# Performance work log

Hardware: AMD Instinct MI355X
Metric: run time of the kernel (lower is better)

Reference implementation:

```python
import jax, jax.numpy as jnp
import numpy as np

D_MODEL = 1024
N_HEADS = 16
HEAD_DIM = D_MODEL // N_HEADS


def setup_inputs() -> dict:
    key = jax.random.key(0)
    ks = jax.random.split(key, 9)
    s = 1.0 / np.sqrt(D_MODEL)
    x = jax.random.normal(ks[0], (2, 2048, D_MODEL), dtype=jnp.float32)
    wq = jax.random.uniform(ks[1], (D_MODEL, D_MODEL), jnp.float32, -s, s)
    bq = jax.random.uniform(ks[2], (D_MODEL,), jnp.float32, -s, s)
    wk = jax.random.uniform(ks[3], (D_MODEL, D_MODEL), jnp.float32, -s, s)
    bk = jax.random.uniform(ks[4], (D_MODEL,), jnp.float32, -s, s)
    wv = jax.random.uniform(ks[5], (D_MODEL, D_MODEL), jnp.float32, -s, s)
    bv = jax.random.uniform(ks[6], (D_MODEL,), jnp.float32, -s, s)
    wo = jax.random.uniform(ks[7], (D_MODEL, D_MODEL), jnp.float32, -s, s)
    bo = jax.random.uniform(ks[8], (D_MODEL,), jnp.float32, -s, s)
    return {"x": x, "wq": wq, "bq": bq, "wk": wk, "bk": bk,
            "wv": wv, "bv": bv, "wo": wo, "bo": bo}


def reference(x, wq, bq, wk, bk, wv, bv, wo, bo):
    B, S, _ = x.shape
    scale = HEAD_DIM ** -0.5

    def proj(w, b):
        # torch Linear: x @ W^T + b, then split heads -> [B, H, S, Dh]
        y = jnp.einsum('bsd,ed->bse', x, w) + b
        return y.reshape(B, S, N_HEADS, HEAD_DIM).transpose(0, 2, 1, 3)

    q = proj(wq, bq)
    k = proj(wk, bk)
    v = proj(wv, bv)

    attn = jnp.einsum('bhqd,bhkd->bhqk', q, k) * scale  # [B,H,S,S]
    causal = jnp.triu(jnp.ones((S, S), dtype=bool), k=1)
    attn = jnp.where(causal, -jnp.inf, attn)
    attn = jax.nn.softmax(attn, axis=-1)
    out = jnp.einsum('bhqk,bhkd->bhqd', attn, v)
    out = out.transpose(0, 2, 1, 3).reshape(B, S, D_MODEL)
    return jnp.einsum('bsd,ed->bse', out, wo) + bo
```

## Files before the change

### kernel.cpp

```cpp
#include <hip/hip_runtime.h>
#include <hip/hip_bf16.h>

#define D_MODEL 1024
#define NHEADS  16
#define HDIM    64
#define SEQ     2048
#define BATCH   2
#define MROWS   (BATCH * SEQ)
#define CHELEM  ((size_t)BATCH * NHEADS * SEQ * HDIM)

typedef __bf16 bf16x8 __attribute__((ext_vector_type(8)));
typedef float  f32x4  __attribute__((ext_vector_type(4)));

__device__ __forceinline__ unsigned short f2bf(float f) {
  unsigned u = __builtin_bit_cast(unsigned, f);
  return (unsigned short)((u + 0x7fffu + ((u >> 16) & 1u)) >> 16);
}

__device__ __forceinline__ float fexp2(float x) {
#if __has_builtin(__builtin_amdgcn_exp2f)
  return __builtin_amdgcn_exp2f(x);
#else
  return __expf(x * 0.6931471805599453f);
#endif
}

__device__ __forceinline__ f32x4 mfma16(bf16x8 a, bf16x8 b, f32x4 c) {
  return __builtin_amdgcn_mfma_f32_16x16x32_bf16(a, b, c, 0, 0, 0);
}

__device__ __forceinline__ void gll16(const unsigned short* g, unsigned short* l) {
  __builtin_amdgcn_global_load_lds(
      (const __attribute__((address_space(1))) unsigned*)g,
      (__attribute__((address_space(3))) unsigned*)l, 16, 0, 0);
}

__global__ void cvt_f32_bf16(const float* __restrict__ in,
                             unsigned short* __restrict__ out, int n4) {
  int i = blockIdx.x * blockDim.x + threadIdx.x;
  if (i >= n4) return;
  float4 v = reinterpret_cast<const float4*>(in)[i];
  ushort4 o;
  o.x = f2bf(v.x); o.y = f2bf(v.y); o.z = f2bf(v.z); o.w = f2bf(v.w);
  reinterpret_cast<ushort4*>(out)[i] = o;
}

__global__ void cvt_w4(const float* __restrict__ s0, const float* __restrict__ s1,
                       const float* __restrict__ s2, const float* __restrict__ s3,
                       unsigned short* __restrict__ d0, unsigned short* __restrict__ d1,
                       unsigned short* __restrict__ d2, unsigned short* __restrict__ d3) {
  int i = blockIdx.x * blockDim.x + threadIdx.x;
  const int y = blockIdx.y;
  const float* s = (y == 0) ? s0 : (y == 1) ? s1 : (y == 2) ? s2 : s3;
  unsigned short* d = (y == 0) ? d0 : (y == 1) ? d1 : (y == 2) ? d2 : d3;
  float4 v = reinterpret_cast<const float4*>(s)[i];
  ushort4 o;
  o.x = f2bf(v.x); o.y = f2bf(v.y); o.z = f2bf(v.z); o.w = f2bf(v.w);
  reinterpret_cast<ushort4*>(d)[i] = o;
}

template <int MODE>
__global__ __launch_bounds__(256) void gemm_bt2(
    const unsigned short* __restrict__ A,
    const unsigned short* __restrict__ Bt,
    const float* __restrict__ b0, const float* __restrict__ b1,
    const float* __restrict__ b2,
    void* __restrict__ outp, int M, int N, int K) {
  __shared__ __align__(16) unsigned short lA[128 * 32];
  __shared__ __align__(16) unsigned short lB[128 * 32];
  const int tid = threadIdx.x;
  const int m0 = blockIdx.y * 128, n0 = blockIdx.x * 128;
  const int lane = tid & 63, wid = tid >> 6;
  const int wr = wid >> 1, wc = wid & 1;
  const int fr = lane & 15, g = lane >> 4;

  const int srow = wid * 32 + (lane >> 2);
  const int scol = ((lane & 3) ^ ((lane >> 3) & 3)) * 8;
  const unsigned short* gA = A + (size_t)(m0 + srow) * K + scol;
  const unsigned short* gB = Bt + (size_t)(n0 + srow) * K + scol;
  unsigned short* lAw = lA + wid * 1024;
  unsigned short* lBw = lB + wid * 1024;

  const int rswz = (g ^ ((fr >> 1) & 3)) * 8;

  f32x4 acc[4][4];
#pragma unroll
  for (int i = 0; i < 4; ++i)
#pragma unroll
    for (int j = 0; j < 4; ++j) acc[i][j] = (f32x4){0.f, 0.f, 0.f, 0.f};

  for (int kt = 0; kt < K; kt += 32) {
    gll16(gA + kt, lAw);
    gll16(gA + (size_t)16 * K + kt, lAw + 512);
    gll16(gB + kt, lBw);
    gll16(gB + (size_t)16 * K + kt, lBw + 512);
    __syncthreads();
    bf16x8 af[4], bfv[4];
#pragma unroll
    for (int i = 0; i < 4; ++i)
      af[i] = *reinterpret_cast<const bf16x8*>(
          &lA[(wr * 64 + i * 16 + fr) * 32 + rswz]);
#pragma unroll
    for (int j = 0; j < 4; ++j)
      bfv[j] = *reinterpret_cast<const bf16x8*>(
          &lB[(wc * 64 + j * 16 + fr) * 32 + rswz]);
#pragma unroll
    for (int i = 0; i < 4; ++i)
#pragma unroll
      for (int j = 0; j < 4; ++j)
        acc[i][j] = mfma16(af[i], bfv[j], acc[i][j]);
    __syncthreads();
  }

  const int src = n0 >> 10;
  const float* bp = (MODE == 2) ? b0 : (src == 0 ? b0 : (src == 1 ? b1 : b2));
#pragma unroll
  for (int i = 0; i < 4; ++i)
#pragma unroll
    for (int j = 0; j < 4; ++j)
#pragma unroll
      for (int r = 0; r < 4; ++r) {
        int m = m0 + wr * 64 + i * 16 + g * 4 + r;
        int n = n0 + wc * 64 + j * 16 + fr;
        if (MODE == 2) {
          float val = acc[i][j][r] + bp[n];
          reinterpret_cast<float*>(outp)[(size_t)m * N + n] = val;
        } else {
          int within = n & 1023;
          float val = acc[i][j][r] + bp[within];
          if (src == 0) val *= 0.1803368867f;
          int b = m >> 11, s = m & 2047;
          int hh = within >> 6, dh = within & 63;
          size_t idx;
          if (src != 2)
            idx = ((size_t)(b * NHEADS + hh) * SEQ + s) * HDIM + dh;
          else
            idx = ((size_t)(b * NHEADS + hh) * HDIM + dh) * SEQ + s;
          reinterpret_cast<unsigned short*>(outp)[(size_t)src * CHELEM + idx] =
              f2bf(val);
        }
      }
}

__global__ __launch_bounds__(256) void attn_fwd12(
    const unsigned short* __restrict__ Q,
    const unsigned short* __restrict__ Km,
    const unsigned short* __restrict__ Vt,
    unsigned short* __restrict__ O) {
  const int tid = threadIdx.x;
  const int lane = tid & 63, wid = tid >> 6;
  const int fr = lane & 15, g = lane >> 4;
  const int lin = blockIdx.x;
  const int c = lin & 7;
  const int t = lin >> 3;
  const int j = t & 15;
  const int sgrp = t >> 4;
  const int slab = sgrp * 8 + c;
  const int b = slab >> 4, h = slab & 15;
  const int bh = b * NHEADS + h;

  __shared__ __align__(16) unsigned short lK[2][4096];
  __shared__ __align__(16) unsigned short lV[2][4096];

  const unsigned short* kptr = Km + (size_t)bh * SEQ * HDIM;
  const unsigned short* vptr = Vt + (size_t)bh * HDIM * SEQ;

  const int sr0 = tid >> 3;
  const int sch = tid & 7;
  const int schx = ((sch ^ (sr0 & 7)) << 3);
  const int kswz0 = ((g ^ (fr & 7)) << 3);
  const int kswz1 = (((4 + g) ^ (fr & 7)) << 3);
  const int g2 = g >> 1, gh = (g & 1) * 4;
  const int vlo0 = (((0 + g2) ^ (fr & 7)) << 3) + gh;
  const int vhi0 = (((2 + g2) ^ (fr & 7)) << 3) + gh;
  const int vlo1 = (((4 + g2) ^ (fr & 7)) << 3) + gh;
  const int vhi1 = (((6 + g2) ^ (fr & 7)) << 3) + gh;

#define STAGE(BI, N0)                                                       \
  { gll16(kptr + (size_t)((N0) + sr0) * HDIM + schx, &lK[BI][wid * 512]);   \
    gll16(kptr + (size_t)((N0) + sr0 + 32) * HDIM + schx,                   \
          &lK[BI][2048 + wid * 512]);                                       \
    gll16(vptr + (size_t)sr0 * SEQ + (N0) + schx, &lV[BI][wid * 512]);      \
    gll16(vptr + (size_t)(sr0 + 32) * SEQ + (N0) + schx,                    \
          &lV[BI][2048 + wid * 512]); }

#pragma unroll 1
  for (int pass = 0; pass < 2; ++pass) {
    const int qt = pass ? (124 - 4 * j + wid) : (4 * j + wid);
    const int q0 = qt * 16;
    const int nkt = pass ? (32 - j) : (j + 1);
    const int qg = q0 + fr;

    const unsigned short* qb = Q + ((size_t)bh * SEQ + qg) * HDIM + g * 8;
    bf16x8 qa0 = *reinterpret_cast<const bf16x8*>(qb);
    bf16x8 qa1 = *reinterpret_cast<const bf16x8*>(qb + 32);

    f32x4 oacc[4];
#pragma unroll
    for (int i = 0; i < 4; ++i) oacc[i] = (f32x4){0.f, 0.f, 0.f, 0.f};
    float mreg = -3e30f;
    float lrow = 0.f;

    STAGE(0, 0);
    __syncthreads();

    for (int kt = 0; kt < nkt; ++kt) {
      const int bi = kt & 1;
      if (kt + 1 < nkt) STAGE(bi ^ 1, (kt + 1) * 64);
      const int n0 = kt * 64;
      bf16x8 kf0[4], kf1[4];
#pragma unroll
      for (int cc = 0; cc < 4; ++cc) {
        kf0[cc] = *reinterpret_cast<const bf16x8*>(
            &lK[bi][(cc * 16 + fr) * 64 + kswz0]);
        kf1[cc] = *reinterpret_cast<const bf16x8*>(
            &lK[bi][(cc * 16 + fr) * 64 + kswz1]);
      }
      f32x4 s[4];
#pragma unroll
      for (int cc = 0; cc < 4; ++cc) {
        s[cc] = (f32x4){0.f, 0.f, 0.f, 0.f};
        s[cc] = mfma16(kf0[cc], qa0, s[cc]);
        s[cc] = mfma16(kf1[cc], qa1, s[cc]);
      }
      float sv[4][4];
      float lmax = -3e30f;
      if (kt == nkt - 1) {
#pragma unroll
        for (int cc = 0; cc < 4; ++cc)
#pragma unroll
          for (int r = 0; r < 4; ++r) {
            sv[cc][r] =
                (n0 + cc * 16 + g * 4 + r <= qg) ? s[cc][r] : -1e30f;
            lmax = fmaxf(lmax, sv[cc][r]);
          }
      } else {
#pragma unroll
        for (int cc = 0; cc < 4; ++cc)
#pragma unroll
          for (int r = 0; r < 4; ++r) {
            sv[cc][r] = s[cc][r];
            lmax = fmaxf(lmax, sv[cc][r]);
          }
      }
      if (!__all(lmax - mreg <= 11.5f)) {
        float tm = lmax;
        tm = fmaxf(tm, __shfl_xor(tm, 16, 64));
        tm = fmaxf(tm, __shfl_xor(tm, 32, 64));
        const float mn = fmaxf(mreg, tm);
        const float al = fexp2(mreg - mn);
        mreg = mn;
        lrow *= al;
#pragma unroll
        for (int nf = 0; nf < 4; ++nf) oacc[nf] *= al;
      }
      union { __bf16 e[8]; bf16x8 v; } pk0, pk1;
#pragma unroll
      for (int r = 0; r < 4; ++r) {
        float p0 = fexp2(sv[0][r] - mreg);
        float p1 = fexp2(sv[1][r] - mreg);
        float p2 = fexp2(sv[2][r] - mreg);
        float p3 = fexp2(sv[3][r] - mreg);
        lrow += (p0 + p1) + (p2 + p3);
        pk0.e[r] = (__bf16)p0; pk0.e[4 + r] = (__bf16)p1;
        pk1.e[r] = (__bf16)p2; pk1.e[4 + r] = (__bf16)p3;
      }
#pragma unroll
      for (int nf = 0; nf < 4; ++nf) {
        const int vrow = (nf * 16 + fr) * 64;
        union { unsigned long long d[2]; bf16x8 v; } v0, v1;
        v0.d[0] = *reinterpret_cast<const unsigned long long*>(&lV[bi][vrow + vlo0]);
        v0.d[1] = *reinterpret_cast<const unsigned long long*>(&lV[bi][vrow + vhi0]);
        v1.d[0] = *reinterpret_cast<const unsigned long long*>(&lV[bi][vrow + vlo1]);
        v1.d[1] = *reinterpret_cast<const unsigned long long*>(&lV[bi][vrow + vhi1]);
        oacc[nf] = mfma16(v0.v, pk0.v, oacc[nf]);
        oacc[nf] = mfma16(v1.v, pk1.v, oacc[nf]);
      }
      __syncthreads();
    }

    float ls = lrow;
    ls += __shfl_xor(ls, 16, 64);
    ls += __shfl_xor(ls, 32, 64);
    const float inv = 1.f / ls;
    const size_t obase = ((size_t)b * SEQ + qg) * D_MODEL + h * HDIM + g * 4;
#pragma unroll
    for (int nf = 0; nf < 4; ++nf) {
      ushort4 o4;
      o4.x = f2bf(oacc[nf][0] * inv);
      o4.y = f2bf(oacc[nf][1] * inv);
      o4.z = f2bf(oacc[nf][2] * inv);
      o4.w = f2bf(oacc[nf][3] * inv);
      *reinterpret_cast<ushort4*>(&O[obase + nf * 16]) = o4;
    }
  }
#undef STAGE
}

extern "C" void kernel_launch(void* const* d_in, const int* in_sizes, int n_in,
                              void* d_out, int out_size, void* d_ws,
                              size_t ws_size, hipStream_t stream) {
  const float* x  = (const float*)d_in[0];
  const float* wq = (const float*)d_in[1];
  const float* bq = (const float*)d_in[2];
  const float* wk = (const float*)d_in[3];
  const float* bk = (const float*)d_in[4];
  const float* wv = (const float*)d_in[5];
  const float* bv = (const float*)d_in[6];
  const float* wo = (const float*)d_in[7];
  const float* bo = (const float*)d_in[8];
  float* out = (float*)d_out;

  char* w = (char*)d_ws;
  unsigned short* xb    = (unsigned short*)w; w += (size_t)MROWS * D_MODEL * 2;
  unsigned short* wqkvb = (unsigned short*)w; w += (size_t)3 * D_MODEL * D_MODEL * 2;
  unsigned short* wob   = (unsigned short*)w; w += (size_t)D_MODEL * D_MODEL * 2;
  unsigned short* Qb    = (unsigned short*)w; w += CHELEM * 2 * 3;
  unsigned short* Ob    = (unsigned short*)w; w += (size_t)MROWS * D_MODEL * 2;
  unsigned short* Kb  = Qb + CHELEM;
  unsigned short* Vtb = Qb + 2 * CHELEM;

  {
    int n4 = MROWS * D_MODEL / 4;
    cvt_f32_bf16<<<n4 / 256, 256, 0, stream>>>(x, xb, n4);
  }
  {
    int n4 = D_MODEL * D_MODEL / 4;
    cvt_w4<<<dim3(n4 / 256, 4), 256, 0, stream>>>(
        wq, wk, wv, wo, wqkvb, wqkvb + (size_t)D_MODEL * D_MODEL,
        wqkvb + (size_t)2 * D_MODEL * D_MODEL, wob);
  }

  gemm_bt2<3><<<dim3(3 * D_MODEL / 128, MROWS / 128), 256, 0, stream>>>(
      xb, wqkvb, bq, bk, bv, Qb, MROWS, 3 * D_MODEL, D_MODEL);

  attn_fwd12<<<512, 256, 0, stream>>>(Qb, Kb, Vtb, Ob);

  gemm_bt2<2><<<dim3(D_MODEL / 128, MROWS / 128), 256, 0, stream>>>(
      Ob, wob, bo, bo, bo, out, MROWS, D_MODEL, D_MODEL);
}
```

Measured before the change: 126.7 us.

## Split KV loop across two wave groups per block and merge softmax partials

Result: slower. 130.0 us (+2.6%).

```diff
diff --git a/kernel.cpp b/kernel.cpp
--- a/kernel.cpp
+++ b/kernel.cpp
@@ -142,7 +142,7 @@
       }
 }
 
-__global__ __launch_bounds__(256) void attn_fwd12(
+__global__ __launch_bounds__(512) void attn_fwd13(
     const unsigned short* __restrict__ Q,
     const unsigned short* __restrict__ Km,
     const unsigned short* __restrict__ Vt,
@@ -150,6 +150,7 @@
   const int tid = threadIdx.x;
   const int lane = tid & 63, wid = tid >> 6;
   const int fr = lane & 15, g = lane >> 4;
+  const int rho = wid >> 2, qsel = wid & 3;
   const int lin = blockIdx.x;
   const int c = lin & 7;
   const int t = lin >> 3;
@@ -159,15 +160,14 @@
   const int b = slab >> 4, h = slab & 15;
   const int bh = b * NHEADS + h;
 
-  __shared__ __align__(16) unsigned short lK[2][4096];
-  __shared__ __align__(16) unsigned short lV[2][4096];
+  __shared__ __align__(16) unsigned short lsm[32768];
 
   const unsigned short* kptr = Km + (size_t)bh * SEQ * HDIM;
   const unsigned short* vptr = Vt + (size_t)bh * HDIM * SEQ;
 
-  const int sr0 = tid >> 3;
+  const int sr = tid >> 3;
   const int sch = tid & 7;
-  const int schx = ((sch ^ (sr0 & 7)) << 3);
+  const int schx = ((sch ^ (sr & 7)) << 3);
   const int kswz0 = ((g ^ (fr & 7)) << 3);
   const int kswz1 = (((4 + g) ^ (fr & 7)) << 3);
   const int g2 = g >> 1, gh = (g & 1) * 4;
@@ -176,19 +176,19 @@
   const int vlo1 = (((4 + g2) ^ (fr & 7)) << 3) + gh;
   const int vhi1 = (((6 + g2) ^ (fr & 7)) << 3) + gh;
 
-#define STAGE(BI, N0)                                                       \
-  { gll16(kptr + (size_t)((N0) + sr0) * HDIM + schx, &lK[BI][wid * 512]);   \
-    gll16(kptr + (size_t)((N0) + sr0 + 32) * HDIM + schx,                   \
-          &lK[BI][2048 + wid * 512]);                                       \
-    gll16(vptr + (size_t)sr0 * SEQ + (N0) + schx, &lV[BI][wid * 512]);      \
-    gll16(vptr + (size_t)(sr0 + 32) * SEQ + (N0) + schx,                    \
-          &lV[BI][2048 + wid * 512]); }
+#define STAGE1(S, SUB, KT)                                                  \
+  { const int n0s = (KT) * 64;                                              \
+    gll16(kptr + (size_t)(n0s + sr) * HDIM + schx,                          \
+          &lsm[(S) * 16384 + (SUB) * 4096 + wid * 512]);                    \
+    gll16(vptr + (size_t)sr * SEQ + n0s + schx,                             \
+          &lsm[(S) * 16384 + 8192 + (SUB) * 4096 + wid * 512]); }
 
 #pragma unroll 1
   for (int pass = 0; pass < 2; ++pass) {
-    const int qt = pass ? (124 - 4 * j + wid) : (4 * j + wid);
+    const int qt = pass ? (124 - 4 * j + qsel) : (4 * j + qsel);
     const int q0 = qt * 16;
     const int nkt = pass ? (32 - j) : (j + 1);
+    const int ni = (nkt + 1) >> 1;
     const int qg = q0 + fr;
 
     const unsigned short* qb = Q + ((size_t)bh * SEQ + qg) * HDIM + g * 8;
@@ -201,100 +201,132 @@
     float mreg = -3e30f;
     float lrow = 0.f;
 
-    STAGE(0, 0);
+    STAGE1(0, 0, 0);
+    if (1 < nkt) STAGE1(0, 1, 1);
     __syncthreads();
 
-    for (int kt = 0; kt < nkt; ++kt) {
-      const int bi = kt & 1;
-      if (kt + 1 < nkt) STAGE(bi ^ 1, (kt + 1) * 64);
-      const int n0 = kt * 64;
-      bf16x8 kf0[4], kf1[4];
-#pragma unroll
-      for (int cc = 0; cc < 4; ++cc) {
-        kf0[cc] = *reinterpret_cast<const bf16x8*>(
-            &lK[bi][(cc * 16 + fr) * 64 + kswz0]);
-        kf1[cc] = *reinterpret_cast<const bf16x8*>(
-            &lK[bi][(cc * 16 + fr) * 64 + kswz1]);
-      }
-      f32x4 s[4];
-#pragma unroll
-      for (int cc = 0; cc < 4; ++cc) {
-        s[cc] = (f32x4){0.f, 0.f, 0.f, 0.f};
-        s[cc] = mfma16(kf0[cc], qa0, s[cc]);
-        s[cc] = mfma16(kf1[cc], qa1, s[cc]);
-      }
-      float sv[4][4];
-      float lmax = -3e30f;
-      if (kt == nkt - 1) {
-#pragma unroll
-        for (int cc = 0; cc < 4; ++cc)
-#pragma unroll
-          for (int r = 0; r < 4; ++r) {
-            sv[cc][r] =
-                (n0 + cc * 16 + g * 4 + r <= qg) ? s[cc][r] : -1e30f;
-            lmax = fmaxf(lmax, sv[cc][r]);
-          }
-      } else {
-#pragma unroll
-        for (int cc = 0; cc < 4; ++cc)
-#pragma unroll
-          for (int r = 0; r < 4; ++r) {
-            sv[cc][r] = s[cc][r];
-            lmax = fmaxf(lmax, sv[cc][r]);
-          }
-      }
-      if (!__all(lmax - mreg <= 11.5f)) {
-        float tm = lmax;
-        tm = fmaxf(tm, __shfl_xor(tm, 16, 64));
-        tm = fmaxf(tm, __shfl_xor(tm, 32, 64));
-        const float mn = fmaxf(mreg, tm);
-        const float al = fexp2(mreg - mn);
-        mreg = mn;
-        lrow *= al;
-#pragma unroll
-        for (int nf = 0; nf < 4; ++nf) oacc[nf] *= al;
-      }
-      union { __bf16 e[8]; bf16x8 v; } pk0, pk1;
-#pragma unroll
-      for (int r = 0; r < 4; ++r) {
-        float p0 = fexp2(sv[0][r] - mreg);
-        float p1 = fexp2(sv[1][r] - mreg);
-        float p2 = fexp2(sv[2][r] - mreg);
-        float p3 = fexp2(sv[3][r] - mreg);
-        lrow += (p0 + p1) + (p2 + p3);
-        pk0.e[r] = (__bf16)p0; pk0.e[4 + r] = (__bf16)p1;
-        pk1.e[r] = (__bf16)p2; pk1.e[4 + r] = (__bf16)p3;
-      }
-#pragma unroll
-      for (int nf = 0; nf < 4; ++nf) {
-        const int vrow = (nf * 16 + fr) * 64;
-        union { unsigned long long d[2]; bf16x8 v; } v0, v1;
-        v0.d[0] = *reinterpret_cast<const unsigned long long*>(&lV[bi][vrow + vlo0]);
-        v0.d[1] = *reinterpret_cast<const unsigned long long*>(&lV[bi][vrow + vhi0]);
-        v1.d[0] = *reinterpret_cast<const unsigned long long*>(&lV[bi][vrow + vlo1]);
-        v1.d[1] = *reinterpret_cast<const unsigned long long*>(&lV[bi][vrow + vhi1]);
-        oacc[nf] = mfma16(v0.v, pk0.v, oacc[nf]);
-        oacc[nf] = mfma16(v1.v, pk1.v, oacc[nf]);
+    for (int i = 0; i < ni; ++i) {
+      const int s = i & 1;
+      if (2 * (i + 1) < nkt) STAGE1(s ^ 1, 0, 2 * (i + 1));
+      if (2 * (i + 1) + 1 < nkt) STAGE1(s ^ 1, 1, 2 * (i + 1) + 1);
+      const int kt = 2 * i + rho;
+      if (kt < nkt) {
+        const int n0 = kt * 64;
+        const unsigned short* Kb = &lsm[s * 16384 + rho * 4096];
+        const unsigned short* Vb = &lsm[s * 16384 + 8192 + rho * 4096];
+        bf16x8 kf0[4], kf1[4];
+#pragma unroll
+        for (int cc = 0; cc < 4; ++cc) {
+          kf0[cc] = *reinterpret_cast<const bf16x8*>(
+              &Kb[(cc * 16 + fr) * 64 + kswz0]);
+          kf1[cc] = *reinterpret_cast<const bf16x8*>(
+              &Kb[(cc * 16 + fr) * 64 + kswz1]);
+        }
+        f32x4 sacc[4];
+#pragma unroll
+        for (int cc = 0; cc < 4; ++cc) {
+          sacc[cc] = (f32x4){0.f, 0.f, 0.f, 0.f};
+          sacc[cc] = mfma16(kf0[cc], qa0, sacc[cc]);
+          sacc[cc] = mfma16(kf1[cc], qa1, sacc[cc]);
+        }
+        float sv[4][4];
+        float lmax = -3e30f;
+        if (kt == nkt - 1) {
+#pragma unroll
+          for (int cc = 0; cc < 4; ++cc)
+#pragma unroll
+            for (int r = 0; r < 4; ++r) {
+              sv[cc][r] =
+                  (n0 + cc * 16 + g * 4 + r <= qg) ? sacc[cc][r] : -1e30f;
+              lmax = fmaxf(lmax, sv[cc][r]);
+            }
+        } else {
+#pragma unroll
+          for (int cc = 0; cc < 4; ++cc)
+#pragma unroll
+            for (int r = 0; r < 4; ++r) {
+              sv[cc][r] = sacc[cc][r];
+              lmax = fmaxf(lmax, sv[cc][r]);
+            }
+        }
+        if (!__all(lmax - mreg <= 11.5f)) {
+          float tm = lmax;
+          tm = fmaxf(tm, __shfl_xor(tm, 16, 64));
+          tm = fmaxf(tm, __shfl_xor(tm, 32, 64));
+          const float mn = fmaxf(mreg, tm);
+          const float al = fexp2(mreg - mn);
+          mreg = mn;
+          lrow *= al;
+#pragma unroll
+          for (int nf = 0; nf < 4; ++nf) oacc[nf] *= al;
+        }
+        union { __bf16 e[8]; bf16x8 v; } pk0, pk1;
+#pragma unroll
+        for (int r = 0; r < 4; ++r) {
+          float p0 = fexp2(sv[0][r] - mreg);
+          float p1 = fexp2(sv[1][r] - mreg);
+          float p2 = fexp2(sv[2][r] - mreg);
+          float p3 = fexp2(sv[3][r] - mreg);
+          lrow += (p0 + p1) + (p2 + p3);
+          pk0.e[r] = (__bf16)p0; pk0.e[4 + r] = (__bf16)p1;
+          pk1.e[r] = (__bf16)p2; pk1.e[4 + r] = (__bf16)p3;
+        }
+#pragma unroll
+        for (int nf = 0; nf < 4; ++nf) {
+          const int vrow = (nf * 16 + fr) * 64;
+          union { unsigned long long d[2]; bf16x8 v; } v0, v1;
+          v0.d[0] = *reinterpret_cast<const unsigned long long*>(&Vb[vrow + vlo0]);
+          v0.d[1] = *reinterpret_cast<const unsigned long long*>(&Vb[vrow + vhi0]);
+          v1.d[0] = *reinterpret_cast<const unsigned long long*>(&Vb[vrow + vlo1]);
+          v1.d[1] = *reinterpret_cast<const unsigned long long*>(&Vb[vrow + vhi1]);
+          oacc[nf] = mfma16(v0.v, pk0.v, oacc[nf]);
+          oacc[nf] = mfma16(v1.v, pk1.v, oacc[nf]);
+        }
       }
       __syncthreads();
     }
 
-    float ls = lrow;
-    ls += __shfl_xor(ls, 16, 64);
-    ls += __shfl_xor(ls, 32, 64);
-    const float inv = 1.f / ls;
-    const size_t obase = ((size_t)b * SEQ + qg) * D_MODEL + h * HDIM + g * 4;
-#pragma unroll
-    for (int nf = 0; nf < 4; ++nf) {
-      ushort4 o4;
-      o4.x = f2bf(oacc[nf][0] * inv);
-      o4.y = f2bf(oacc[nf][1] * inv);
-      o4.z = f2bf(oacc[nf][2] * inv);
-      o4.w = f2bf(oacc[nf][3] * inv);
-      *reinterpret_cast<ushort4*>(&O[obase + nf * 16]) = o4;
+    {
+      char* mb = reinterpret_cast<char*>(lsm);
+      const int moff = qsel * 5120 + lane * 80;
+      if (rho == 1) {
+#pragma unroll
+        for (int nf = 0; nf < 4; ++nf)
+          *reinterpret_cast<f32x4*>(mb + moff + nf * 16) = oacc[nf];
+        *reinterpret_cast<float*>(mb + moff + 64) = mreg;
+        *reinterpret_cast<float*>(mb + moff + 68) = lrow;
+      }
+      __syncthreads();
+      if (rho == 0) {
+        f32x4 oB[4];
+#pragma unroll
+        for (int nf = 0; nf < 4; ++nf)
+          oB[nf] = *reinterpret_cast<const f32x4*>(mb + moff + nf * 16);
+        const float mB = *reinterpret_cast<const float*>(mb + moff + 64);
+        const float lB = *reinterpret_cast<const float*>(mb + moff + 68);
+        const float M = fmaxf(mreg, mB);
+        const float aA = fexp2(mreg - M);
+        const float aB = fexp2(mB - M);
+        float lsum = lrow * aA + lB * aB;
+        lsum += __shfl_xor(lsum, 16, 64);
+        lsum += __shfl_xor(lsum, 32, 64);
+        const float inv = 1.f / lsum;
+        const size_t obase =
+            ((size_t)b * SEQ + qg) * D_MODEL + h * HDIM + g * 4;
+#pragma unroll
+        for (int nf = 0; nf < 4; ++nf) {
+          ushort4 o4;
+          o4.x = f2bf((oacc[nf][0] * aA + oB[nf][0] * aB) * inv);
+          o4.y = f2bf((oacc[nf][1] * aA + oB[nf][1] * aB) * inv);
+          o4.z = f2bf((oacc[nf][2] * aA + oB[nf][2] * aB) * inv);
+          o4.w = f2bf((oacc[nf][3] * aA + oB[nf][3] * aB) * inv);
+          *reinterpret_cast<ushort4*>(&O[obase + nf * 16]) = o4;
+        }
+      }
+      __syncthreads();
     }
   }
-#undef STAGE
+#undef STAGE1
 }
 
 extern "C" void kernel_launch(void* const* d_in, const int* in_sizes, int n_in,
@@ -334,7 +366,7 @@
   gemm_bt2<3><<<dim3(3 * D_MODEL / 128, MROWS / 128), 256, 0, stream>>>(
       xb, wqkvb, bq, bk, bv, Qb, MROWS, 3 * D_MODEL, D_MODEL);
 
-  attn_fwd12<<<512, 256, 0, stream>>>(Qb, Kb, Vtb, Ob);
+  attn_fwd13<<<512, 512, 0, stream>>>(Qb, Kb, Vtb, Ob);
 
   gemm_bt2<2><<<dim3(D_MODEL / 128, MROWS / 128), 256, 0, stream>>>(
       Ob, wob, bo, bo, bo, out, MROWS, D_MODEL, D_MODEL);
```
